# Kernel tuning notes

Measured on AMD Instinct MI355X. Metric: run time of the kernel, lower is better.

The kernel has to match this reference:

```python
import jax, jax.numpy as jnp
import numpy as np

B, IN, E, HID, OUT = 16384, 256, 32, 64, 128


def setup_inputs() -> dict:
    key = jax.random.key(0)
    ks = jax.random.split(key, 14)
    s = 0.05
    return {
        "x": jax.random.normal(ks[0], (B, IN), dtype=jnp.float32),
        "Wg": jax.random.normal(ks[1], (IN, E), dtype=jnp.float32) * s,
        "bg": jnp.zeros((E,), dtype=jnp.float32),
        "W1": jax.random.normal(ks[2], (E, IN, HID), dtype=jnp.float32) * s,
        "b1": jnp.zeros((E, HID), dtype=jnp.float32),
        "W2": jax.random.normal(ks[3], (E, HID, 256), dtype=jnp.float32) * s,
        "b2": jnp.zeros((E, 256), dtype=jnp.float32),
        "W3": jax.random.normal(ks[4], (E, 256, 128), dtype=jnp.float32) * s,
        "b3": jnp.zeros((E, 128), dtype=jnp.float32),
        "W4": jax.random.normal(ks[5], (E, 128, HID), dtype=jnp.float32) * s,
        "b4": jnp.zeros((E, HID), dtype=jnp.float32),
        "W5": jax.random.normal(ks[6], (E, HID, OUT), dtype=jnp.float32) * s,
        "b5": jnp.zeros((E, OUT), dtype=jnp.float32),
    }


def reference(x, Wg, bg, W1, b1, W2, b2, W3, b3, W4, b4, W5, b5):
    # Gating: softmax over experts. [B, E]
    g = jax.nn.softmax(x @ Wg + bg, axis=1)
    # All experts evaluated densely via batched GEMMs (fused expert axis).
    h = jax.nn.relu(jnp.einsum('bi,eih->beh', x, W1) + b1)   # [B,E,64]
    h = jax.nn.relu(jnp.einsum('beh,ehm->bem', h, W2) + b2)  # [B,E,256]
    # Dropout(0.2) is identity in eval mode.
    h = jax.nn.relu(jnp.einsum('bem,emn->ben', h, W3) + b3)  # [B,E,128]
    h = jax.nn.relu(jnp.einsum('ben,enh->beh', h, W4) + b4)  # [B,E,64]
    y = jnp.einsum('beh,eho->beo', h, W5) + b5               # [B,E,OUT]
    # Gating-weighted sum over experts: einsum('bi,bij->bj').
    return jnp.einsum('be,beo->bo', g, y)
```

## Files before the change

kernel.cpp:

```cpp
#include <hip/hip_runtime.h>

#define BB      16384
#define IN_DIM  256
#define NE      32
#define H1D     64
#define H2D     256
#define H3D     128
#define NOUT    128

typedef __bf16 bf16_t;
typedef __bf16 bf16x4_t __attribute__((ext_vector_type(4)));
typedef __bf16 bf16x8  __attribute__((ext_vector_type(8)));
typedef float  f32x4   __attribute__((ext_vector_type(4)));

#define OFF_WF   ((size_t)0)
#define OFF_WGF  ((size_t)NE * 81920 * 2)

__global__ __launch_bounds__(256) void build_frags(
    const float* __restrict__ W1, const float* __restrict__ W2,
    const float* __restrict__ W3, const float* __restrict__ W4,
    const float* __restrict__ W5, const float* __restrict__ Wg,
    bf16_t* __restrict__ Wf, bf16_t* __restrict__ Wgf)
{
    const int g    = blockIdx.x * 256 + threadIdx.x;
    const int lane = g & 63;
    const int set  = g >> 6;
    const float* src; bf16_t* dst; int N, t, ks;
    if (set < 5120) {
        const int e = set / 160;
        const int s = set % 160;
        dst = Wf + (size_t)e * 81920 + ((size_t)s * 64 + lane) * 8;
        if (s < 32)       { t = s >> 3;         ks = s & 7;         N = 64;  src = W1 + (size_t)e * 16384; }
        else if (s < 64)  { t = (s - 32) >> 1;  ks = (s - 32) & 1;  N = 256; src = W2 + (size_t)e * 16384; }
        else if (s < 128) { t = (s - 64) >> 3;  ks = (s - 64) & 7;  N = 128; src = W3 + (size_t)e * 32768; }
        else if (s < 144) { t = (s - 128) >> 2; ks = (s - 128) & 3; N = 64;  src = W4 + (size_t)e * 8192;  }
        else              { t = (s - 144) >> 1; ks = (s - 144) & 1; N = 128; src = W5 + (size_t)e * 8192;  }
    } else {
        const int s = set - 5120;
        t = s >> 3; ks = s & 7; N = 32; src = Wg;
        dst = Wgf + ((size_t)s * 64 + lane) * 8;
    }
    const int f  = t * 16 + (lane & 15);
    const int k0 = ks * 32 + (lane >> 4) * 8;
    bf16x8 o;
#pragma unroll
    for (int j = 0; j < 8; j++) o[j] = (bf16_t)src[(size_t)(k0 + j) * N + f];
    *(bf16x8*)dst = o;
}

template<int RS>
__device__ __forceinline__ void* swzp(char* base, int row, int byteoff) {
    const int g = byteoff >> 4;
    return (void*)(base + ((row << RS) | ((g ^ (row & 7)) << 4) | (byteoff & 15)));
}

#define L_H1   0
#define L_SX   8192
#define L_H2   40960
#define L_H3   73728
#define L_H4   90112
#define L_SG   98304
#define L_TOT  106496

__global__ __launch_bounds__(512) void moe_main(
    const float* __restrict__ x, const bf16_t* __restrict__ Wf,
    const bf16_t* __restrict__ Wgf, const float* __restrict__ bg,
    const float* __restrict__ b1, const float* __restrict__ b2,
    const float* __restrict__ b3, const float* __restrict__ b4,
    const float* __restrict__ b5, float* __restrict__ out)
{
    __shared__ __align__(16) char lds[L_TOT];
    char* sX = lds + L_SX;
    char* h1 = lds + L_H1;
    char* h2 = lds + L_H2;
    char* h3 = lds + L_H3;
    char* h4 = lds + L_H4;
    float* sG = (float*)(lds + L_SG);

    const int tid  = threadIdx.x;
    const int w    = tid >> 6;
    const int lane = tid & 63;
    const int c    = lane & 15;
    const int q    = lane >> 4;
    const int fg   = w & 3;
    const int mh   = w >> 2;
    const int b0   = blockIdx.x * 64;

    bf16x8 wA[8], wB[2][2], wC[8], wD[4], wE[2];

#pragma unroll
    for (int ks = 0; ks < 8; ks++)
        wA[ks] = *(const bf16x8*)(Wf + ((size_t)(fg * 8 + ks) * 64 + lane) * 8);
#pragma unroll
    for (int nt = 0; nt < 2; nt++)
#pragma unroll
        for (int ks = 0; ks < 2; ks++)
            wB[nt][ks] = *(const bf16x8*)(Wf + 16384 + ((size_t)((w * 2 + nt) * 2 + ks) * 64 + lane) * 8);

    {
        const int r  = tid >> 3;
        const int c0 = (tid & 7) * 32;
        const float* sp = x + (size_t)(b0 + r) * IN_DIM + c0;
#pragma unroll
        for (int jj = 0; jj < 4; jj++) {
            const float4 v0 = *(const float4*)(sp + jj * 8);
            const float4 v1 = *(const float4*)(sp + jj * 8 + 4);
            bf16x8 o = { (bf16_t)v0.x, (bf16_t)v0.y, (bf16_t)v0.z, (bf16_t)v0.w,
                         (bf16_t)v1.x, (bf16_t)v1.y, (bf16_t)v1.z, (bf16_t)v1.w };
            *(bf16x8*)swzp<9>(sX, r, c0 * 2 + jj * 16) = o;
        }
    }
    __syncthreads();

    {
        const int t = w & 1, m = w >> 1;
        f32x4 acc = (f32x4){0.f, 0.f, 0.f, 0.f};
#pragma unroll
        for (int ks = 0; ks < 8; ks++) {
            bf16x8 xv = *(const bf16x8*)swzp<9>(sX, m * 16 + c, ks * 64 + q * 16);
            bf16x8 wg = *(const bf16x8*)(Wgf + ((size_t)(t * 8 + ks) * 64 + lane) * 8);
            acc = __builtin_amdgcn_mfma_f32_16x16x32_bf16(wg, xv, acc, 0, 0, 0);
        }
        const float4 bgv = *(const float4*)(bg + t * 16 + q * 4);
        float* sLgF = (float*)h3;
        *(float4*)(sLgF + (size_t)(m * 16 + c) * 36 + t * 16 + q * 4) =
            (float4){acc[0] + bgv.x, acc[1] + bgv.y, acc[2] + bgv.z, acc[3] + bgv.w};
    }
    __syncthreads();

    {
        const int r = tid >> 3;
        const int j = tid & 7;
        const float* sLgF = (const float*)h3;
        float4 l = *(const float4*)(sLgF + (size_t)r * 36 + j * 4);
        float mx = fmaxf(fmaxf(l.x, l.y), fmaxf(l.z, l.w));
#pragma unroll
        for (int off = 1; off < 8; off <<= 1) mx = fmaxf(mx, __shfl_xor(mx, off));
        float e0 = __expf(l.x - mx), e1 = __expf(l.y - mx),
              e2 = __expf(l.z - mx), e3 = __expf(l.w - mx);
        float sm = e0 + e1 + e2 + e3;
#pragma unroll
        for (int off = 1; off < 8; off <<= 1) sm += __shfl_xor(sm, off);
        const float rs = 1.f / sm;
        sG[(j * 4 + 0) * 64 + r] = e0 * rs;
        sG[(j * 4 + 1) * 64 + r] = e1 * rs;
        sG[(j * 4 + 2) * 64 + r] = e2 * rs;
        sG[(j * 4 + 3) * 64 + r] = e3 * rs;
    }
    {
        const float4 bv = *(const float4*)(b1 + fg * 16 + q * 4);
#pragma unroll
        for (int mm = 0; mm < 2; mm++) {
            const int m = mh * 2 + mm;
            f32x4 acc = (f32x4){0.f, 0.f, 0.f, 0.f};
#pragma unroll
            for (int ks = 0; ks < 8; ks++) {
                bf16x8 xv = *(const bf16x8*)swzp<9>(sX, m * 16 + c, ks * 64 + q * 16);
                acc = __builtin_amdgcn_mfma_f32_16x16x32_bf16(wA[ks], xv, acc, 0, 0, 0);
            }
            bf16x4_t hv = { (bf16_t)fmaxf(acc[0] + bv.x, 0.f),
                            (bf16_t)fmaxf(acc[1] + bv.y, 0.f),
                            (bf16_t)fmaxf(acc[2] + bv.z, 0.f),
                            (bf16_t)fmaxf(acc[3] + bv.w, 0.f) };
            *(bf16x4_t*)swzp<7>(h1, m * 16 + c, fg * 32 + q * 8) = hv;
        }
    }
    __syncthreads();

    float oacc[4][4];
#pragma unroll
    for (int m = 0; m < 4; m++)
#pragma unroll
        for (int r = 0; r < 4; r++) oacc[m][r] = 0.f;

    auto do_l5 = [&](int ep) {
        const float4 bv = *(const float4*)(b5 + (size_t)ep * NOUT + w * 16 + q * 4);
#pragma unroll
        for (int m = 0; m < 4; m++) {
            f32x4 acc = (f32x4){0.f, 0.f, 0.f, 0.f};
#pragma unroll
            for (int ks = 0; ks < 2; ks++) {
                bf16x8 ha = *(const bf16x8*)swzp<7>(h4, m * 16 + c, ks * 64 + q * 16);
                acc = __builtin_amdgcn_mfma_f32_16x16x32_bf16(wE[ks], ha, acc, 0, 0, 0);
            }
            const float gv = sG[ep * 64 + m * 16 + c];
            oacc[m][0] += gv * (acc[0] + bv.x);
            oacc[m][1] += gv * (acc[1] + bv.y);
            oacc[m][2] += gv * (acc[2] + bv.z);
            oacc[m][3] += gv * (acc[3] + bv.w);
        }
    };

    auto do_l4 = [&](int ep) {
        const float4 bv = *(const float4*)(b4 + (size_t)ep * H1D + fg * 16 + q * 4);
#pragma unroll
        for (int mm = 0; mm < 2; mm++) {
            const int m = mh * 2 + mm;
            f32x4 acc = (f32x4){0.f, 0.f, 0.f, 0.f};
#pragma unroll
            for (int ks = 0; ks < 4; ks++) {
                bf16x8 ha = *(const bf16x8*)swzp<8>(h3, m * 16 + c, ks * 64 + q * 16);
                acc = __builtin_amdgcn_mfma_f32_16x16x32_bf16(wD[ks], ha, acc, 0, 0, 0);
            }
            bf16x4_t hv = { (bf16_t)fmaxf(acc[0] + bv.x, 0.f),
                            (bf16_t)fmaxf(acc[1] + bv.y, 0.f),
                            (bf16_t)fmaxf(acc[2] + bv.z, 0.f),
                            (bf16_t)fmaxf(acc[3] + bv.w, 0.f) };
            *(bf16x4_t*)swzp<7>(h4, m * 16 + c, fg * 32 + q * 8) = hv;
        }
    };

    for (int e = 0; e < NE; e++) {
        const bf16_t* We  = Wf + (size_t)e * 81920;
        const bf16_t* Wen = Wf + (size_t)((e + 1) & 31) * 81920;
        const bf16_t* Wep = Wf + (size_t)((e - 1) & 31) * 81920;

#pragma unroll
        for (int ks = 0; ks < 8; ks++)
            wC[ks] = *(const bf16x8*)(We + 32768 + ((size_t)(w * 8 + ks) * 64 + lane) * 8);
#pragma unroll
        for (int ks = 0; ks < 8; ks++)
            wA[ks] = *(const bf16x8*)(Wen + ((size_t)(fg * 8 + ks) * 64 + lane) * 8);

        {
            float4 bv[2];
#pragma unroll
            for (int nt = 0; nt < 2; nt++)
                bv[nt] = *(const float4*)(b2 + (size_t)e * H2D + (w * 2 + nt) * 16 + q * 4);
#pragma unroll
            for (int m = 0; m < 4; m++) {
                bf16x8 ha[2];
#pragma unroll
                for (int ks = 0; ks < 2; ks++)
                    ha[ks] = *(const bf16x8*)swzp<7>(h1, m * 16 + c, ks * 64 + q * 16);
                f32x4 acc[2];
#pragma unroll
                for (int nt = 0; nt < 2; nt++) acc[nt] = (f32x4){0.f, 0.f, 0.f, 0.f};
#pragma unroll
                for (int nt = 0; nt < 2; nt++)
#pragma unroll
                    for (int ks = 0; ks < 2; ks++)
                        acc[nt] = __builtin_amdgcn_mfma_f32_16x16x32_bf16(wB[nt][ks], ha[ks], acc[nt], 0, 0, 0);
#pragma unroll
                for (int nt = 0; nt < 2; nt++) {
                    bf16x4_t hv = { (bf16_t)fmaxf(acc[nt][0] + bv[nt].x, 0.f),
                                    (bf16_t)fmaxf(acc[nt][1] + bv[nt].y, 0.f),
                                    (bf16_t)fmaxf(acc[nt][2] + bv[nt].z, 0.f),
                                    (bf16_t)fmaxf(acc[nt][3] + bv[nt].w, 0.f) };
                    *(bf16x4_t*)swzp<9>(h2, m * 16 + c, (w * 2 + nt) * 32 + q * 8) = hv;
                }
            }
        }
        if (e > 0) do_l4(e - 1);
        __syncthreads();

        if (e > 0) {
#pragma unroll
            for (int ks = 0; ks < 2; ks++)
                wE[ks] = *(const bf16x8*)(Wep + 73728 + ((size_t)(w * 2 + ks) * 64 + lane) * 8);
        }
#pragma unroll
        for (int nt = 0; nt < 2; nt++)
#pragma unroll
            for (int ks = 0; ks < 2; ks++)
                wB[nt][ks] = *(const bf16x8*)(Wen + 16384 + ((size_t)((w * 2 + nt) * 2 + ks) * 64 + lane) * 8);
#pragma unroll
        for (int ks = 0; ks < 4; ks++)
            wD[ks] = *(const bf16x8*)(We + 65536 + ((size_t)(fg * 4 + ks) * 64 + lane) * 8);

        {
            const float4 bv = *(const float4*)(b3 + (size_t)e * H3D + w * 16 + q * 4);
#pragma unroll
            for (int m = 0; m < 4; m++) {
                f32x4 acc = (f32x4){0.f, 0.f, 0.f, 0.f};
#pragma unroll
                for (int ks = 0; ks < 8; ks++) {
                    bf16x8 ha = *(const bf16x8*)swzp<9>(h2, m * 16 + c, ks * 64 + q * 16);
                    acc = __builtin_amdgcn_mfma_f32_16x16x32_bf16(wC[ks], ha, acc, 0, 0, 0);
                }
                bf16x4_t hv = { (bf16_t)fmaxf(acc[0] + bv.x, 0.f),
                                (bf16_t)fmaxf(acc[1] + bv.y, 0.f),
                                (bf16_t)fmaxf(acc[2] + bv.z, 0.f),
                                (bf16_t)fmaxf(acc[3] + bv.w, 0.f) };
                *(bf16x4_t*)swzp<8>(h3, m * 16 + c, w * 32 + q * 8) = hv;
            }
        }
        if (e < NE - 1) {
            const float4 bv = *(const float4*)(b1 + (size_t)(e + 1) * H1D + fg * 16 + q * 4);
#pragma unroll
            for (int mm = 0; mm < 2; mm++) {
                const int m = mh * 2 + mm;
                f32x4 acc = (f32x4){0.f, 0.f, 0.f, 0.f};
#pragma unroll
                for (int ks = 0; ks < 8; ks++) {
                    bf16x8 xv = *(const bf16x8*)swzp<9>(sX, m * 16 + c, ks * 64 + q * 16);
                    acc = __builtin_amdgcn_mfma_f32_16x16x32_bf16(wA[ks], xv, acc, 0, 0, 0);
                }
                bf16x4_t hv = { (bf16_t)fmaxf(acc[0] + bv.x, 0.f),
                                (bf16_t)fmaxf(acc[1] + bv.y, 0.f),
                                (bf16_t)fmaxf(acc[2] + bv.z, 0.f),
                                (bf16_t)fmaxf(acc[3] + bv.w, 0.f) };
                *(bf16x4_t*)swzp<7>(h1, m * 16 + c, fg * 32 + q * 8) = hv;
            }
        }
        if (e > 0) do_l5(e - 1);
        __syncthreads();
    }

#pragma unroll
    for (int ks = 0; ks < 2; ks++)
        wE[ks] = *(const bf16x8*)(Wf + (size_t)31 * 81920 + 73728 + ((size_t)(w * 2 + ks) * 64 + lane) * 8);
    do_l4(NE - 1);
    __syncthreads();
    do_l5(NE - 1);

#pragma unroll
    for (int m = 0; m < 4; m++)
        *(float4*)(out + (size_t)(b0 + m * 16 + c) * NOUT + w * 16 + q * 4) =
            (float4){oacc[m][0], oacc[m][1], oacc[m][2], oacc[m][3]};
}

extern "C" void kernel_launch(void* const* d_in, const int* in_sizes, int n_in,
                              void* d_out, int out_size, void* d_ws, size_t ws_size,
                              hipStream_t stream)
{
    (void)in_sizes; (void)n_in; (void)out_size; (void)ws_size;
    const float* x  = (const float*)d_in[0];
    const float* Wg = (const float*)d_in[1];
    const float* bg = (const float*)d_in[2];
    const float* W1 = (const float*)d_in[3];
    const float* b1 = (const float*)d_in[4];
    const float* W2 = (const float*)d_in[5];
    const float* b2 = (const float*)d_in[6];
    const float* W3 = (const float*)d_in[7];
    const float* b3 = (const float*)d_in[8];
    const float* W4 = (const float*)d_in[9];
    const float* b4 = (const float*)d_in[10];
    const float* W5 = (const float*)d_in[11];
    const float* b5 = (const float*)d_in[12];

    char* ws = (char*)d_ws;
    bf16_t* Wf  = (bf16_t*)(ws + OFF_WF);
    bf16_t* Wgf = (bf16_t*)(ws + OFF_WGF);
    float*  outp = (float*)d_out;

    build_frags<<<dim3(1284), dim3(256), 0, stream>>>(W1, W2, W3, W4, W5, Wg, Wf, Wgf);
    moe_main<<<dim3(BB / 64), dim3(512), 0, stream>>>(x, Wf, Wgf, bg,
                                                      b1, b2, b3, b4, b5, outp);
}
```

Before: 226.3 us.

## Use 32x32x16 MFMA tiles for expert layers 2, 3 and 5

Moves the weight fragment layout for W2, W3 and W5 to a 32-wide output tile with K split in steps of 16. Layers 2, 3 and 5 switch from 16x16x32 to 32x32x16 bf16 MFMA instructions, with each wave owning a 32-row by 32-column output block. Larger tiles halve the number of LDS activation reads per output and cut MFMA issue count. In exchange each wave holds more weight registers (wC grows to 16 fragments) and 16-wide accumulators, which raises register pressure.

```diff
diff --git a/kernel.cpp b/kernel.cpp
--- a/kernel.cpp
+++ b/kernel.cpp
@@ -12,6 +12,7 @@
 typedef __bf16 bf16x4_t __attribute__((ext_vector_type(4)));
 typedef __bf16 bf16x8  __attribute__((ext_vector_type(8)));
 typedef float  f32x4   __attribute__((ext_vector_type(4)));
+typedef float  f32x16  __attribute__((ext_vector_type(16)));
 
 #define OFF_WF   ((size_t)0)
 #define OFF_WGF  ((size_t)NE * 81920 * 2)
@@ -25,23 +26,24 @@
     const int g    = blockIdx.x * 256 + threadIdx.x;
     const int lane = g & 63;
     const int set  = g >> 6;
-    const float* src; bf16_t* dst; int N, t, ks;
+    const float* src; bf16_t* dst; int N, t, ks; bool big;
     if (set < 5120) {
         const int e = set / 160;
         const int s = set % 160;
         dst = Wf + (size_t)e * 81920 + ((size_t)s * 64 + lane) * 8;
-        if (s < 32)       { t = s >> 3;         ks = s & 7;         N = 64;  src = W1 + (size_t)e * 16384; }
-        else if (s < 64)  { t = (s - 32) >> 1;  ks = (s - 32) & 1;  N = 256; src = W2 + (size_t)e * 16384; }
-        else if (s < 128) { t = (s - 64) >> 3;  ks = (s - 64) & 7;  N = 128; src = W3 + (size_t)e * 32768; }
-        else if (s < 144) { t = (s - 128) >> 2; ks = (s - 128) & 3; N = 64;  src = W4 + (size_t)e * 8192;  }
-        else              { t = (s - 144) >> 1; ks = (s - 144) & 1; N = 128; src = W5 + (size_t)e * 8192;  }
+        if (s < 32)       { t = s >> 3;            ks = s & 7;          N = 64;  big = false; src = W1 + (size_t)e * 16384; }
+        else if (s < 64)  { int r = s - 32;  t = r >> 2;  ks = r & 3;   N = 256; big = true;  src = W2 + (size_t)e * 16384; }
+        else if (s < 128) { int r = s - 64;  t = r >> 4;  ks = r & 15;  N = 128; big = true;  src = W3 + (size_t)e * 32768; }
+        else if (s < 144) { int r = s - 128; t = r >> 2;  ks = r & 3;   N = 64;  big = false; src = W4 + (size_t)e * 8192;  }
+        else              { int r = s - 144; t = r >> 2;  ks = r & 3;   N = 128; big = true;  src = W5 + (size_t)e * 8192;  }
     } else {
         const int s = set - 5120;
-        t = s >> 3; ks = s & 7; N = 32; src = Wg;
+        t = s >> 3; ks = s & 7; N = 32; big = false; src = Wg;
         dst = Wgf + ((size_t)s * 64 + lane) * 8;
     }
-    const int f  = t * 16 + (lane & 15);
-    const int k0 = ks * 32 + (lane >> 4) * 8;
+    int f, k0;
+    if (big) { f = t * 32 + (lane & 31); k0 = ks * 16 + (lane >> 5) * 8; }
+    else     { f = t * 16 + (lane & 15); k0 = ks * 32 + (lane >> 4) * 8; }
     bf16x8 o;
 #pragma unroll
     for (int j = 0; j < 8; j++) o[j] = (bf16_t)src[(size_t)(k0 + j) * N + f];
@@ -82,20 +84,23 @@
     const int lane = tid & 63;
     const int c    = lane & 15;
     const int q    = lane >> 4;
+    const int c2   = lane & 31;
+    const int h    = lane >> 5;
     const int fg   = w & 3;
     const int mh   = w >> 2;
+    const int bb   = mh * 32 + c2;
     const int b0   = blockIdx.x * 64;
 
-    bf16x8 wA[8], wB[2][2], wC[8], wD[4], wE[2];
+    bf16x8 wA[8], wB[2][4], wC[16], wD[4], wE[4];
 
 #pragma unroll
     for (int ks = 0; ks < 8; ks++)
         wA[ks] = *(const bf16x8*)(Wf + ((size_t)(fg * 8 + ks) * 64 + lane) * 8);
 #pragma unroll
-    for (int nt = 0; nt < 2; nt++)
-#pragma unroll
-        for (int ks = 0; ks < 2; ks++)
-            wB[nt][ks] = *(const bf16x8*)(Wf + 16384 + ((size_t)((w * 2 + nt) * 2 + ks) * 64 + lane) * 8);
+    for (int jt = 0; jt < 2; jt++)
+#pragma unroll
+        for (int ks = 0; ks < 4; ks++)
+            wB[jt][ks] = *(const bf16x8*)(Wf + ((size_t)(32 + (fg * 2 + jt) * 4 + ks) * 64 + lane) * 8);
 
     {
         const int r  = tid >> 3;
@@ -167,27 +172,27 @@
     }
     __syncthreads();
 
-    float oacc[4][4];
-#pragma unroll
-    for (int m = 0; m < 4; m++)
-#pragma unroll
-        for (int r = 0; r < 4; r++) oacc[m][r] = 0.f;
+    float oacc[16];
+#pragma unroll
+    for (int r = 0; r < 16; r++) oacc[r] = 0.f;
 
     auto do_l5 = [&](int ep) {
-        const float4 bv = *(const float4*)(b5 + (size_t)ep * NOUT + w * 16 + q * 4);
-#pragma unroll
-        for (int m = 0; m < 4; m++) {
-            f32x4 acc = (f32x4){0.f, 0.f, 0.f, 0.f};
-#pragma unroll
-            for (int ks = 0; ks < 2; ks++) {
-                bf16x8 ha = *(const bf16x8*)swzp<7>(h4, m * 16 + c, ks * 64 + q * 16);
-                acc = __builtin_amdgcn_mfma_f32_16x16x32_bf16(wE[ks], ha, acc, 0, 0, 0);
-            }
-            const float gv = sG[ep * 64 + m * 16 + c];
-            oacc[m][0] += gv * (acc[0] + bv.x);
-            oacc[m][1] += gv * (acc[1] + bv.y);
-            oacc[m][2] += gv * (acc[2] + bv.z);
-            oacc[m][3] += gv * (acc[3] + bv.w);
+        f32x16 p;
+#pragma unroll
+        for (int r = 0; r < 16; r++) p[r] = 0.f;
+#pragma unroll
+        for (int ks = 0; ks < 4; ks++) {
+            bf16x8 ha = *(const bf16x8*)swzp<7>(h4, bb, ks * 32 + h * 16);
+            p = __builtin_amdgcn_mfma_f32_32x32x16_bf16(wE[ks], ha, p, 0, 0, 0);
+        }
+        const float gv = sG[ep * 64 + bb];
+#pragma unroll
+        for (int t = 0; t < 4; t++) {
+            const float4 bv = *(const float4*)(b5 + (size_t)ep * NOUT + fg * 32 + t * 8 + h * 4);
+            oacc[4 * t + 0] += gv * (p[4 * t + 0] + bv.x);
+            oacc[4 * t + 1] += gv * (p[4 * t + 1] + bv.y);
+            oacc[4 * t + 2] += gv * (p[4 * t + 2] + bv.z);
+            oacc[4 * t + 3] += gv * (p[4 * t + 3] + bv.w);
         }
     };
 
@@ -216,38 +221,38 @@
         const bf16_t* Wep = Wf + (size_t)((e - 1) & 31) * 81920;
 
 #pragma unroll
-        for (int ks = 0; ks < 8; ks++)
-            wC[ks] = *(const bf16x8*)(We + 32768 + ((size_t)(w * 8 + ks) * 64 + lane) * 8);
+        for (int ks = 0; ks < 16; ks++)
+            wC[ks] = *(const bf16x8*)(We + ((size_t)(64 + fg * 16 + ks) * 64 + lane) * 8);
 #pragma unroll
         for (int ks = 0; ks < 8; ks++)
             wA[ks] = *(const bf16x8*)(Wen + ((size_t)(fg * 8 + ks) * 64 + lane) * 8);
 
         {
-            float4 bv[2];
-#pragma unroll
-            for (int nt = 0; nt < 2; nt++)
-                bv[nt] = *(const float4*)(b2 + (size_t)e * H2D + (w * 2 + nt) * 16 + q * 4);
-#pragma unroll
-            for (int m = 0; m < 4; m++) {
-                bf16x8 ha[2];
-#pragma unroll
-                for (int ks = 0; ks < 2; ks++)
-                    ha[ks] = *(const bf16x8*)swzp<7>(h1, m * 16 + c, ks * 64 + q * 16);
-                f32x4 acc[2];
-#pragma unroll
-                for (int nt = 0; nt < 2; nt++) acc[nt] = (f32x4){0.f, 0.f, 0.f, 0.f};
-#pragma unroll
-                for (int nt = 0; nt < 2; nt++)
-#pragma unroll
-                    for (int ks = 0; ks < 2; ks++)
-                        acc[nt] = __builtin_amdgcn_mfma_f32_16x16x32_bf16(wB[nt][ks], ha[ks], acc[nt], 0, 0, 0);
-#pragma unroll
-                for (int nt = 0; nt < 2; nt++) {
-                    bf16x4_t hv = { (bf16_t)fmaxf(acc[nt][0] + bv[nt].x, 0.f),
-                                    (bf16_t)fmaxf(acc[nt][1] + bv[nt].y, 0.f),
-                                    (bf16_t)fmaxf(acc[nt][2] + bv[nt].z, 0.f),
-                                    (bf16_t)fmaxf(acc[nt][3] + bv[nt].w, 0.f) };
-                    *(bf16x4_t*)swzp<9>(h2, m * 16 + c, (w * 2 + nt) * 32 + q * 8) = hv;
+            bf16x8 ha[4];
+#pragma unroll
+            for (int ks = 0; ks < 4; ks++)
+                ha[ks] = *(const bf16x8*)swzp<7>(h1, bb, ks * 32 + h * 16);
+            f32x16 acc[2];
+#pragma unroll
+            for (int jt = 0; jt < 2; jt++)
+#pragma unroll
+                for (int r = 0; r < 16; r++) acc[jt][r] = 0.f;
+#pragma unroll
+            for (int jt = 0; jt < 2; jt++)
+#pragma unroll
+                for (int ks = 0; ks < 4; ks++)
+                    acc[jt] = __builtin_amdgcn_mfma_f32_32x32x16_bf16(wB[jt][ks], ha[ks], acc[jt], 0, 0, 0);
+#pragma unroll
+            for (int jt = 0; jt < 2; jt++) {
+                const int ft = fg * 2 + jt;
+#pragma unroll
+                for (int t = 0; t < 4; t++) {
+                    const float4 bv = *(const float4*)(b2 + (size_t)e * H2D + ft * 32 + t * 8 + h * 4);
+                    bf16x4_t hv = { (bf16_t)fmaxf(acc[jt][4 * t + 0] + bv.x, 0.f),
+                                    (bf16_t)fmaxf(acc[jt][4 * t + 1] + bv.y, 0.f),
+                                    (bf16_t)fmaxf(acc[jt][4 * t + 2] + bv.z, 0.f),
+                                    (bf16_t)fmaxf(acc[jt][4 * t + 3] + bv.w, 0.f) };
+                    *(bf16x4_t*)swzp<9>(h2, bb, ft * 64 + t * 16 + h * 8) = hv;
                 }
             }
         }
@@ -256,33 +261,35 @@
 
         if (e > 0) {
 #pragma unroll
-            for (int ks = 0; ks < 2; ks++)
-                wE[ks] = *(const bf16x8*)(Wep + 73728 + ((size_t)(w * 2 + ks) * 64 + lane) * 8);
-        }
-#pragma unroll
-        for (int nt = 0; nt < 2; nt++)
-#pragma unroll
-            for (int ks = 0; ks < 2; ks++)
-                wB[nt][ks] = *(const bf16x8*)(Wen + 16384 + ((size_t)((w * 2 + nt) * 2 + ks) * 64 + lane) * 8);
+            for (int ks = 0; ks < 4; ks++)
+                wE[ks] = *(const bf16x8*)(Wep + ((size_t)(144 + fg * 4 + ks) * 64 + lane) * 8);
+        }
+#pragma unroll
+        for (int jt = 0; jt < 2; jt++)
+#pragma unroll
+            for (int ks = 0; ks < 4; ks++)
+                wB[jt][ks] = *(const bf16x8*)(Wen + ((size_t)(32 + (fg * 2 + jt) * 4 + ks) * 64 + lane) * 8);
 #pragma unroll
         for (int ks = 0; ks < 4; ks++)
-            wD[ks] = *(const bf16x8*)(We + 65536 + ((size_t)(fg * 4 + ks) * 64 + lane) * 8);
+            wD[ks] = *(const bf16x8*)(We + ((size_t)(128 + fg * 4 + ks) * 64 + lane) * 8);
 
         {
-            const float4 bv = *(const float4*)(b3 + (size_t)e * H3D + w * 16 + q * 4);
-#pragma unroll
-            for (int m = 0; m < 4; m++) {
-                f32x4 acc = (f32x4){0.f, 0.f, 0.f, 0.f};
-#pragma unroll
-                for (int ks = 0; ks < 8; ks++) {
-                    bf16x8 ha = *(const bf16x8*)swzp<9>(h2, m * 16 + c, ks * 64 + q * 16);
-                    acc = __builtin_amdgcn_mfma_f32_16x16x32_bf16(wC[ks], ha, acc, 0, 0, 0);
-                }
-                bf16x4_t hv = { (bf16_t)fmaxf(acc[0] + bv.x, 0.f),
-                                (bf16_t)fmaxf(acc[1] + bv.y, 0.f),
-                                (bf16_t)fmaxf(acc[2] + bv.z, 0.f),
-                                (bf16_t)fmaxf(acc[3] + bv.w, 0.f) };
-                *(bf16x4_t*)swzp<8>(h3, m * 16 + c, w * 32 + q * 8) = hv;
+            f32x16 acc;
+#pragma unroll
+            for (int r = 0; r < 16; r++) acc[r] = 0.f;
+#pragma unroll
+            for (int ks = 0; ks < 16; ks++) {
+                bf16x8 ha = *(const bf16x8*)swzp<9>(h2, bb, ks * 32 + h * 16);
+                acc = __builtin_amdgcn_mfma_f32_32x32x16_bf16(wC[ks], ha, acc, 0, 0, 0);
+            }
+#pragma unroll
+            for (int t = 0; t < 4; t++) {
+                const float4 bv = *(const float4*)(b3 + (size_t)e * H3D + fg * 32 + t * 8 + h * 4);
+                bf16x4_t hv = { (bf16_t)fmaxf(acc[4 * t + 0] + bv.x, 0.f),
+                                (bf16_t)fmaxf(acc[4 * t + 1] + bv.y, 0.f),
+                                (bf16_t)fmaxf(acc[4 * t + 2] + bv.z, 0.f),
+                                (bf16_t)fmaxf(acc[4 * t + 3] + bv.w, 0.f) };
+                *(bf16x4_t*)swzp<8>(h3, bb, fg * 64 + t * 16 + h * 8) = hv;
             }
         }
         if (e < NE - 1) {
@@ -308,16 +315,16 @@
     }
 
 #pragma unroll
-    for (int ks = 0; ks < 2; ks++)
-        wE[ks] = *(const bf16x8*)(Wf + (size_t)31 * 81920 + 73728 + ((size_t)(w * 2 + ks) * 64 + lane) * 8);
+    for (int ks = 0; ks < 4; ks++)
+        wE[ks] = *(const bf16x8*)(Wf + (size_t)31 * 81920 + ((size_t)(144 + fg * 4 + ks) * 64 + lane) * 8);
     do_l4(NE - 1);
     __syncthreads();
     do_l5(NE - 1);
 
 #pragma unroll
-    for (int m = 0; m < 4; m++)
-        *(float4*)(out + (size_t)(b0 + m * 16 + c) * NOUT + w * 16 + q * 4) =
-            (float4){oacc[m][0], oacc[m][1], oacc[m][2], oacc[m][3]};
+    for (int t = 0; t < 4; t++)
+        *(float4*)(out + (size_t)(b0 + bb) * NOUT + fg * 32 + t * 8 + h * 4) =
+            (float4){oacc[4 * t + 0], oacc[4 * t + 1], oacc[4 * t + 2], oacc[4 * t + 3]};
 }
 
 extern "C" void kernel_launch(void* const* d_in, const int* in_sizes, int n_in,
```

Result: slower. 251.4 us (+11.1%).
